# Kernel optimization log

Measured on AMD Instinct MI355X. Metric: run time of the kernel, lower is better.

## Reference

```python
import jax, jax.numpy as jnp
import numpy as np

BLOCK = 128
LN_EPS = 1e-5

def _dequant(W, scale):
    # expand per-128x128-block scales to full weight shape, multiply
    s = jnp.repeat(jnp.repeat(scale, BLOCK, axis=0), BLOCK, axis=1)
    return W * s[:W.shape[0], :W.shape[1]]

def _fp8_linear(x, W, scale):
    # mock fp8 block-scaled linear: y = x @ dequant(W).T
    return jnp.einsum('bsh,oh->bso', x, _dequant(W, scale))

def _layernorm(x, gamma, beta):
    mu = jnp.mean(x, axis=-1, keepdims=True)
    var = jnp.mean(jnp.square(x - mu), axis=-1, keepdims=True)
    return (x - mu) * jax.lax.rsqrt(var + LN_EPS) * gamma + beta

def setup_inputs() -> dict:
    key = jax.random.key(0)
    ks = jax.random.split(key, 8)
    H, L, S = 1024, 4096, 1024
    B, T = 8, 4096
    return {
        'x': jax.random.normal(ks[0], (B, T, H), dtype=jnp.float32),
        'W_large': jax.random.normal(ks[1], (L, H), dtype=jnp.float32),
        'W_s1': jax.random.normal(ks[2], (S, H), dtype=jnp.float32),
        'W_s2': jax.random.normal(ks[3], (S, H), dtype=jnp.float32),
        'W_c1': jax.random.normal(ks[4], (L, L), dtype=jnp.float32) * 0.02,
        'W_c2': jax.random.normal(ks[5], (H, L), dtype=jnp.float32) * 0.02,
        'gamma': jnp.ones((H,), dtype=jnp.float32),
        'beta': jnp.zeros((H,), dtype=jnp.float32),
        's_large': jnp.ones((L // BLOCK, H // BLOCK), dtype=jnp.float32),
        's_s1': jnp.ones((S // BLOCK, H // BLOCK), dtype=jnp.float32),
        's_s2': jnp.ones((S // BLOCK, H // BLOCK), dtype=jnp.float32),
    }

def reference(x, W_large, W_s1, W_s2, W_c1, W_c2, gamma, beta, s_large, s_s1, s_s2):
    H = x.shape[-1]
    big = jax.nn.relu(_fp8_linear(x, W_large, s_large))          # [B,T,L]
    big = jax.nn.relu(jnp.einsum('bsl,ol->bso', big, W_c1))      # [B,T,L]
    big = jnp.einsum('bsl,hl->bsh', big, W_c2)                   # [B,T,H]
    s1 = _fp8_linear(x, W_s1, s_s1)[..., :H]
    s2 = _fp8_linear(x, W_s2, s_s2)[..., :H]
    return _layernorm(big + s1 + s2, gamma, beta)
```

## Files before the change

### kernel.cpp

```cpp
#include <hip/hip_runtime.h>
#include <hip/hip_bf16.h>
#include <stdint.h>


typedef short bf16x8 __attribute__((ext_vector_type(8)));
typedef float f32x4 __attribute__((ext_vector_type(4)));

#define GLOAD_LDS16(g, l)                                                     \
  __builtin_amdgcn_global_load_lds(                                           \
      (const __attribute__((address_space(1))) void*)(g),                     \
      (__attribute__((address_space(3))) void*)(l), 16, 0, 0)

__device__ __forceinline__ ushort f2b(float f) {
  uint32_t u = __builtin_bit_cast(uint32_t, f);
  u += 0x7fffu + ((u >> 16) & 1u);
  return (ushort)(u >> 16);
}

__global__ __launch_bounds__(256) void cvt_scale(
    const float* __restrict__ src, ushort* __restrict__ dst, long n4, int cols,
    const float* __restrict__ scale, int scols) {
  long i = (long)blockIdx.x * blockDim.x + threadIdx.x;
  long stride = (long)gridDim.x * blockDim.x;
  for (; i < n4; i += stride) {
    long e = i * 4;
    float4 v = ((const float4*)src)[i];
    float s = 1.f;
    if (scale) {
      int r = (int)(e / cols), c = (int)(e % cols);
      s = scale[(r >> 7) * scols + (c >> 7)];
    }
    ushort4 o;
    o.x = f2b(v.x * s); o.y = f2b(v.y * s);
    o.z = f2b(v.z * s); o.w = f2b(v.w * s);
    ((ushort4*)dst)[i] = o;
  }
}

__global__ __launch_bounds__(256) void make_wsum(
    const float* __restrict__ W1, const float* __restrict__ s1,
    const float* __restrict__ W2, const float* __restrict__ s2,
    ushort* __restrict__ dst) {
  const long n4 = (1024L * 1024L) / 4;
  long i = (long)blockIdx.x * blockDim.x + threadIdx.x;
  long stride = (long)gridDim.x * blockDim.x;
  for (; i < n4; i += stride) {
    long e = i * 4;
    int r = (int)(e >> 10), c = (int)(e & 1023);
    int si = (r >> 7) * 8 + (c >> 7);
    float f1 = s1[si], f2 = s2[si];
    float4 a = ((const float4*)W1)[i];
    float4 b = ((const float4*)W2)[i];
    ushort4 o;
    o.x = f2b(a.x * f1 + b.x * f2); o.y = f2b(a.y * f1 + b.y * f2);
    o.z = f2b(a.z * f1 + b.z * f2); o.w = f2b(a.w * f1 + b.w * f2);
    ((ushort4*)dst)[i] = o;
  }
}

template <int EPI>
__global__ __launch_bounds__(256, 2) void gemm_bt(
    const ushort* __restrict__ A1, const ushort* __restrict__ B1, int lda1,
    int ldb1, int K1, const ushort* __restrict__ A2,
    const ushort* __restrict__ B2, int lda2, int ldb2, int K2,
    void* __restrict__ Cout, int N) {
  __shared__ __align__(16) ushort As[128 * 32];
  __shared__ __align__(16) ushort Bs[128 * 32];
  const int t = threadIdx.x;
  const int l = t & 63;
  const int w = t >> 6;
  const int wr = w >> 1, wc = w & 1;
  const int fr = l & 15, fq = l >> 4;

  const int n0 = blockIdx.x * 128;
  const int m0 = blockIdx.y * 128;

  f32x4 acc[4][4];
#pragma unroll
  for (int i = 0; i < 4; i++)
#pragma unroll
    for (int j = 0; j < 4; j++) acc[i][j] = (f32x4){0.f, 0.f, 0.f, 0.f};

  const int srow = t >> 2;
  const int scol = (t & 3) * 8;
  const int wbase = (t >> 6) * 1024;

  const int KT = (K1 + K2) >> 5;
  for (int kt = 0; kt < KT; ++kt) {
    const ushort* Ap;
    const ushort* Bp;
    int lda, ldb, k0;
    const int kk = kt << 5;
    if (kk < K1) {
      Ap = A1; Bp = B1; lda = lda1; ldb = ldb1; k0 = kk;
    } else {
      Ap = A2; Bp = B2; lda = lda2; ldb = ldb2; k0 = kk - K1;
    }

    __syncthreads();
#pragma unroll
    for (int c = 0; c < 2; ++c) {
      const ushort* ga = Ap + (size_t)(m0 + c * 64 + srow) * lda + (k0 + scol);
      GLOAD_LDS16(ga, (char*)As + c * 4096 + wbase);
      const ushort* gb = Bp + (size_t)(n0 + c * 64 + srow) * ldb + (k0 + scol);
      GLOAD_LDS16(gb, (char*)Bs + c * 4096 + wbase);
    }
    __syncthreads();

    bf16x8 af[4], bfr[4];
#pragma unroll
    for (int mi = 0; mi < 4; mi++)
      af[mi] = *(const bf16x8*)&As[(wr * 64 + mi * 16 + fr) * 32 + fq * 8];
#pragma unroll
    for (int ni = 0; ni < 4; ni++)
      bfr[ni] = *(const bf16x8*)&Bs[(wc * 64 + ni * 16 + fr) * 32 + fq * 8];
#pragma unroll
    for (int mi = 0; mi < 4; mi++)
#pragma unroll
      for (int ni = 0; ni < 4; ni++)
        acc[mi][ni] = __builtin_amdgcn_mfma_f32_16x16x32_bf16(
            af[mi], bfr[ni], acc[mi][ni], 0, 0, 0);
  }

#pragma unroll
  for (int mi = 0; mi < 4; mi++) {
#pragma unroll
    for (int ni = 0; ni < 4; ni++) {
#pragma unroll
      for (int j = 0; j < 4; j++) {
        const int row = m0 + wr * 64 + mi * 16 + fq * 4 + j;
        const int col = n0 + wc * 64 + ni * 16 + fr;
        const float v = acc[mi][ni][j];
        if (EPI == 0) {
          ((ushort*)Cout)[(size_t)row * N + col] = f2b(fmaxf(v, 0.f));
        } else {
          ((float*)Cout)[(size_t)row * N + col] = v;
        }
      }
    }
  }
}

__global__ __launch_bounds__(256) void ln_inplace(
    float* __restrict__ buf, const float* __restrict__ gamma,
    const float* __restrict__ beta) {
  const int t = threadIdx.x;
  float* row = buf + (size_t)blockIdx.x * 1024;
  float4 v = ((const float4*)row)[t];
  float s = v.x + v.y + v.z + v.w;
  float ss = v.x * v.x + v.y * v.y + v.z * v.z + v.w * v.w;
#pragma unroll
  for (int off = 32; off > 0; off >>= 1) {
    s += __shfl_down(s, off, 64);
    ss += __shfl_down(ss, off, 64);
  }
  __shared__ float red_s[4], red_ss[4];
  if ((t & 63) == 0) {
    red_s[t >> 6] = s;
    red_ss[t >> 6] = ss;
  }
  __syncthreads();
  const float tot = red_s[0] + red_s[1] + red_s[2] + red_s[3];
  const float tot2 = red_ss[0] + red_ss[1] + red_ss[2] + red_ss[3];
  const float mu = tot * (1.f / 1024.f);
  const float var = tot2 * (1.f / 1024.f) - mu * mu;
  const float rs = rsqrtf(var + 1e-5f);
  const float4 g = ((const float4*)gamma)[t];
  const float4 b = ((const float4*)beta)[t];
  float4 o;
  o.x = (v.x - mu) * rs * g.x + b.x;
  o.y = (v.y - mu) * rs * g.y + b.y;
  o.z = (v.z - mu) * rs * g.z + b.z;
  o.w = (v.w - mu) * rs * g.w + b.w;
  ((float4*)row)[t] = o;
}

extern "C" void kernel_launch(void* const* d_in, const int* in_sizes, int n_in,
                              void* d_out, int out_size, void* d_ws,
                              size_t ws_size, hipStream_t stream) {
  const float* x = (const float*)d_in[0];
  const float* W_large = (const float*)d_in[1];
  const float* W_s1 = (const float*)d_in[2];
  const float* W_s2 = (const float*)d_in[3];
  const float* W_c1 = (const float*)d_in[4];
  const float* W_c2 = (const float*)d_in[5];
  const float* gamma = (const float*)d_in[6];
  const float* beta = (const float*)d_in[7];
  const float* s_large = (const float*)d_in[8];
  const float* s_s1 = (const float*)d_in[9];
  const float* s_s2 = (const float*)d_in[10];

  const long BT = 32768;

  char* ws = (char*)d_ws;
  size_t off = 0;
  ushort* Wlb  = (ushort*)(ws + off); off += 4096L * 1024 * 2;
  ushort* Wc1b = (ushort*)(ws + off); off += 4096L * 4096 * 2;
  ushort* Wc2b = (ushort*)(ws + off); off += 1024L * 4096 * 2;
  ushort* Wsb  = (ushort*)(ws + off); off += 1024L * 1024 * 2;
  ushort* xb   = (ushort*)(ws + off); off += BT * 1024 * 2;

  size_t remain = (ws_size > off) ? (ws_size - off) : 0;
  long Mc = (long)(remain / 2 / (4096 * 2));
  Mc = (Mc / 128) * 128;
  if (Mc > BT) Mc = BT;
  if (Mc < 128) Mc = 128;
  ushort* big1 = (ushort*)(ws + off);
  ushort* big2 = big1 + (size_t)Mc * 4096;

  cvt_scale<<<2048, 256, 0, stream>>>(x, xb, BT * 1024 / 4, 1024, nullptr, 0);
  cvt_scale<<<1024, 256, 0, stream>>>(W_large, Wlb, 4194304L / 4, 1024,
                                      s_large, 8);
  cvt_scale<<<2048, 256, 0, stream>>>(W_c1, Wc1b, 16777216L / 4, 4096, nullptr,
                                      0);
  cvt_scale<<<1024, 256, 0, stream>>>(W_c2, Wc2b, 4194304L / 4, 4096, nullptr,
                                      0);
  make_wsum<<<512, 256, 0, stream>>>(W_s1, s_s1, W_s2, s_s2, Wsb);

  for (long m = 0; m < BT; m += Mc) {
    const long mc = (BT - m < Mc) ? (BT - m) : Mc;
    const int mb = (int)(mc / 128);
    const ushort* xc = xb + m * 1024;
    gemm_bt<0><<<dim3(32, mb), 256, 0, stream>>>(
        xc, Wlb, 1024, 1024, 1024, xc, Wlb, 1024, 1024, 0, big1, 4096);
    gemm_bt<0><<<dim3(32, mb), 256, 0, stream>>>(
        big1, Wc1b, 4096, 4096, 4096, big1, Wc1b, 4096, 4096, 0, big2, 4096);
    gemm_bt<1><<<dim3(8, mb), 256, 0, stream>>>(
        big2, Wc2b, 4096, 4096, 4096, xc, Wsb, 1024, 1024, 1024,
        (float*)d_out + m * 1024, 1024);
  }
  ln_inplace<<<(int)BT, 256, 0, stream>>>((float*)d_out, gamma, beta);
}
```

Baseline: 2.423 ms.

## Replace GEMM with 256x256-tile, 8-wave, 4-stage pipelined kernel with XCD swizzle

Rewrites the bf16 GEMM to use 256x256 output tiles computed by 512 threads (8 waves). K-tiles are staged through a four-buffer LDS ring using async global-to-LDS loads with explicit vmcnt waits, so memory traffic overlaps MFMA work. It also adds an XCD-aware block-index swizzle and priority boosting around the MFMA bursts. The aim is to cut global traffic per FLOP and hide load latency. In exchange it needs 128KB of dynamic LDS and hand-tuned wait counts that must stay correct at the pipeline tail.

```diff
diff --git a/kernel.cpp b/kernel.cpp
--- a/kernel.cpp
+++ b/kernel.cpp
@@ -59,76 +59,140 @@
 }
 
 template <int EPI>
-__global__ __launch_bounds__(256, 2) void gemm_bt(
+__global__ __launch_bounds__(512, 2) void gemm8(
     const ushort* __restrict__ A1, const ushort* __restrict__ B1, int lda1,
     int ldb1, int K1, const ushort* __restrict__ A2,
     const ushort* __restrict__ B2, int lda2, int ldb2, int K2,
-    void* __restrict__ Cout, int N) {
-  __shared__ __align__(16) ushort As[128 * 32];
-  __shared__ __align__(16) ushort Bs[128 * 32];
+    void* __restrict__ Cout, int N, int gridN) {
+  extern __shared__ __align__(16) char lds[];
+
   const int t = threadIdx.x;
   const int l = t & 63;
-  const int w = t >> 6;
-  const int wr = w >> 1, wc = w & 1;
+  const int wid = t >> 6;
+  const int wr = wid >> 2;
+  const int wc = wid & 3;
   const int fr = l & 15, fq = l >> 4;
 
-  const int n0 = blockIdx.x * 128;
-  const int m0 = blockIdx.y * 128;
-
-  f32x4 acc[4][4];
-#pragma unroll
-  for (int i = 0; i < 4; i++)
+  const int nwg = gridDim.x;
+  {
+  }
+  int bid = blockIdx.x;
+  const int xcd = bid & 7, idx = bid >> 3;
+  const int q = nwg >> 3, r = nwg & 7;
+  const int swz = ((xcd < r) ? xcd * (q + 1) : r * (q + 1) + (xcd - r) * q) +
+                  idx;
+  const int m0 = (swz / gridN) * 256;
+  const int n0 = (swz % gridN) * 256;
+
+  const int srow = wid * 16 + (l >> 2);
+  const int scol = (l & 3) * 8;
+
+  const int aoff = (wr * 128 + fr) * 64 + fq * 16;
+  const int boff = (wc * 64 + fr) * 64 + fq * 16;
+
+  const int NT = (K1 + K2) >> 5;
+
+  auto stageA = [&](int tt, int sb) {
+    int kk = tt << 5;
+    const ushort* P;
+    int ld;
+    if (kk < K1) {
+      P = A1; ld = lda1;
+    } else {
+      P = A2; ld = lda2; kk -= K1;
+    }
+    const ushort* s0 = P + (size_t)(m0 + srow) * ld + kk + scol;
+    char* d0 = lds + sb * 32768 + wid * 1024;
+    GLOAD_LDS16(s0, d0);
+    GLOAD_LDS16(s0 + (size_t)128 * ld, d0 + 8192);
+  };
+  auto stageB = [&](int tt, int sb) {
+    int kk = tt << 5;
+    const ushort* P;
+    int ld;
+    if (kk < K1) {
+      P = B1; ld = ldb1;
+    } else {
+      P = B2; ld = ldb2; kk -= K1;
+    }
+    const ushort* s0 = P + (size_t)(n0 + srow) * ld + kk + scol;
+    char* d0 = lds + sb * 32768 + 16384 + wid * 1024;
+    GLOAD_LDS16(s0, d0);
+    GLOAD_LDS16(s0 + (size_t)128 * ld, d0 + 8192);
+  };
+
+  f32x4 acc[8][4];
+#pragma unroll
+  for (int i = 0; i < 8; i++)
 #pragma unroll
     for (int j = 0; j < 4; j++) acc[i][j] = (f32x4){0.f, 0.f, 0.f, 0.f};
 
-  const int srow = t >> 2;
-  const int scol = (t & 3) * 8;
-  const int wbase = (t >> 6) * 1024;
-
-  const int KT = (K1 + K2) >> 5;
-  for (int kt = 0; kt < KT; ++kt) {
-    const ushort* Ap;
-    const ushort* Bp;
-    int lda, ldb, k0;
-    const int kk = kt << 5;
-    if (kk < K1) {
-      Ap = A1; Bp = B1; lda = lda1; ldb = ldb1; k0 = kk;
-    } else {
-      Ap = A2; Bp = B2; lda = lda2; ldb = ldb2; k0 = kk - K1;
-    }
-
-    __syncthreads();
-#pragma unroll
-    for (int c = 0; c < 2; ++c) {
-      const ushort* ga = Ap + (size_t)(m0 + c * 64 + srow) * lda + (k0 + scol);
-      GLOAD_LDS16(ga, (char*)As + c * 4096 + wbase);
-      const ushort* gb = Bp + (size_t)(n0 + c * 64 + srow) * ldb + (k0 + scol);
-      GLOAD_LDS16(gb, (char*)Bs + c * 4096 + wbase);
-    }
-    __syncthreads();
-
-    bf16x8 af[4], bfr[4];
-#pragma unroll
-    for (int mi = 0; mi < 4; mi++)
-      af[mi] = *(const bf16x8*)&As[(wr * 64 + mi * 16 + fr) * 32 + fq * 8];
-#pragma unroll
-    for (int ni = 0; ni < 4; ni++)
-      bfr[ni] = *(const bf16x8*)&Bs[(wc * 64 + ni * 16 + fr) * 32 + fq * 8];
-#pragma unroll
-    for (int mi = 0; mi < 4; mi++)
-#pragma unroll
-      for (int ni = 0; ni < 4; ni++)
+  stageA(0, 0); stageB(0, 0);
+  stageA(1, 1); stageB(1, 1);
+  stageA(2, 2); stageB(2, 2);
+  asm volatile("s_waitcnt vmcnt(8)" ::: "memory");
+  __builtin_amdgcn_s_barrier();
+
+  for (int kt = 0; kt < NT; ++kt) {
+    const int b = kt & 3;
+    const char* Ab = lds + b * 32768;
+    const char* Bb = Ab + 16384;
+    const bool sOK = (kt + 3 < NT);
+    const int sb = (kt + 3) & 3;
+
+    bf16x8 bfr[4], af[4];
+#pragma unroll
+    for (int ni = 0; ni < 4; ++ni)
+      bfr[ni] = *(const bf16x8*)(Bb + boff + ni * 1024);
+#pragma unroll
+    for (int mi = 0; mi < 4; ++mi)
+      af[mi] = *(const bf16x8*)(Ab + aoff + mi * 1024);
+    if (sOK) stageA(kt + 3, sb);
+    __builtin_amdgcn_s_barrier();
+    asm volatile("s_waitcnt lgkmcnt(0)" ::: "memory");
+    __builtin_amdgcn_sched_barrier(0);
+    __builtin_amdgcn_s_setprio(1);
+#pragma unroll
+    for (int mi = 0; mi < 4; ++mi)
+#pragma unroll
+      for (int ni = 0; ni < 4; ++ni)
         acc[mi][ni] = __builtin_amdgcn_mfma_f32_16x16x32_bf16(
             af[mi], bfr[ni], acc[mi][ni], 0, 0, 0);
-  }
-
-#pragma unroll
-  for (int mi = 0; mi < 4; mi++) {
-#pragma unroll
-    for (int ni = 0; ni < 4; ni++) {
-#pragma unroll
-      for (int j = 0; j < 4; j++) {
-        const int row = m0 + wr * 64 + mi * 16 + fq * 4 + j;
+    __builtin_amdgcn_s_setprio(0);
+    __builtin_amdgcn_s_barrier();
+
+#pragma unroll
+    for (int mi = 0; mi < 4; ++mi)
+      af[mi] = *(const bf16x8*)(Ab + aoff + (mi + 4) * 1024);
+    if (sOK) stageB(kt + 3, sb);
+    __builtin_amdgcn_s_barrier();
+    asm volatile("s_waitcnt lgkmcnt(0)" ::: "memory");
+    __builtin_amdgcn_sched_barrier(0);
+    __builtin_amdgcn_s_setprio(1);
+#pragma unroll
+    for (int mi = 0; mi < 4; ++mi)
+#pragma unroll
+      for (int ni = 0; ni < 4; ++ni)
+        acc[mi + 4][ni] = __builtin_amdgcn_mfma_f32_16x16x32_bf16(
+            af[mi], bfr[ni], acc[mi + 4][ni], 0, 0, 0);
+    __builtin_amdgcn_s_setprio(0);
+    if (kt + 4 <= NT) {
+      asm volatile("s_waitcnt vmcnt(8)" ::: "memory");
+    } else if (kt + 3 == NT) {
+      asm volatile("s_waitcnt vmcnt(4)" ::: "memory");
+    } else if (kt + 2 == NT) {
+      asm volatile("s_waitcnt vmcnt(0)" ::: "memory");
+    }
+    __builtin_amdgcn_s_barrier();
+  }
+
+#pragma unroll
+  for (int mi = 0; mi < 8; ++mi) {
+#pragma unroll
+    for (int ni = 0; ni < 4; ++ni) {
+#pragma unroll
+      for (int j = 0; j < 4; ++j) {
+        const int row = m0 + wr * 128 + mi * 16 + fq * 4 + j;
         const int col = n0 + wc * 64 + ni * 16 + fr;
         const float v = acc[mi][ni][j];
         if (EPI == 0) {
@@ -202,9 +266,9 @@
 
   size_t remain = (ws_size > off) ? (ws_size - off) : 0;
   long Mc = (long)(remain / 2 / (4096 * 2));
-  Mc = (Mc / 128) * 128;
+  Mc = (Mc / 256) * 256;
   if (Mc > BT) Mc = BT;
-  if (Mc < 128) Mc = 128;
+  if (Mc < 256) Mc = 256;
   ushort* big1 = (ushort*)(ws + off);
   ushort* big2 = big1 + (size_t)Mc * 4096;
 
@@ -217,17 +281,19 @@
                                       0);
   make_wsum<<<512, 256, 0, stream>>>(W_s1, s_s1, W_s2, s_s2, Wsb);
 
+  const int LDS = 131072;
   for (long m = 0; m < BT; m += Mc) {
     const long mc = (BT - m < Mc) ? (BT - m) : Mc;
-    const int mb = (int)(mc / 128);
+    const int mb = (int)(mc / 256);
     const ushort* xc = xb + m * 1024;
-    gemm_bt<0><<<dim3(32, mb), 256, 0, stream>>>(
-        xc, Wlb, 1024, 1024, 1024, xc, Wlb, 1024, 1024, 0, big1, 4096);
-    gemm_bt<0><<<dim3(32, mb), 256, 0, stream>>>(
-        big1, Wc1b, 4096, 4096, 4096, big1, Wc1b, 4096, 4096, 0, big2, 4096);
-    gemm_bt<1><<<dim3(8, mb), 256, 0, stream>>>(
+    gemm8<0><<<mb * 16, 512, LDS, stream>>>(
+        xc, Wlb, 1024, 1024, 1024, xc, Wlb, 1024, 1024, 0, big1, 4096, 16);
+    gemm8<0><<<mb * 16, 512, LDS, stream>>>(
+        big1, Wc1b, 4096, 4096, 4096, big1, Wc1b, 4096, 4096, 0, big2, 4096,
+        16);
+    gemm8<1><<<mb * 4, 512, LDS, stream>>>(
         big2, Wc2b, 4096, 4096, 4096, xc, Wsb, 1024, 1024, 1024,
-        (float*)d_out + m * 1024, 1024);
+        (float*)d_out + m * 1024, 1024, 4);
   }
   ln_inplace<<<(int)BT, 256, 0, stream>>>((float*)d_out, gamma, beta);
 }
```

Measured after the change: 2.279 ms. -5.9%, faster.
